# Kernel tuning notes

Measured on AMD Instinct MI355X. Metric: run time of the kernel, lower is better.

Reference implementation:

```python
import jax, jax.numpy as jnp
import numpy as np

N_NODES = 100_000
N_EDGES = 3_200_000
IN_FEATS, N_HIDDEN, N_CLASSES = 512, 64, 32
ALPHA = 0.1
NITER = 10


def setup_inputs() -> dict:
    key = jax.random.key(0)
    kx, kw1, kw2, kr, kc = jax.random.split(key, 5)
    x = jax.random.normal(kx, (N_NODES, IN_FEATS), dtype=jnp.float32)
    w1 = jax.random.normal(kw1, (N_HIDDEN, IN_FEATS), dtype=jnp.float32) / np.sqrt(IN_FEATS)
    w2 = jax.random.normal(kw2, (N_CLASSES, N_HIDDEN), dtype=jnp.float32) / np.sqrt(N_HIDDEN)
    # random edges + self loops (A + I in calc_A_hat)
    r = jax.random.randint(kr, (N_EDGES,), 0, N_NODES, dtype=jnp.int32)
    c = jax.random.randint(kc, (N_EDGES,), 0, N_NODES, dtype=jnp.int32)
    loop = jnp.arange(N_NODES, dtype=jnp.int32)
    rows = jnp.concatenate([r, loop])
    cols = jnp.concatenate([c, loop])
    # symmetric-normalization values: (1-alpha) / sqrt(d[r]*d[c]); self loops guarantee d>=1
    deg = jax.ops.segment_sum(jnp.ones_like(rows, dtype=jnp.float32), rows, num_segments=N_NODES)
    vals = (1.0 - ALPHA) / jnp.sqrt(deg[rows] * deg[cols])
    return {"x": x, "w1": w1, "w2": w2, "rows": rows, "cols": cols, "vals": vals}


def reference(x, w1, w2, rows, cols, vals):
    n = x.shape[0]
    # 2-layer bias-free MLP (dropout is identity with drop_prob=None)
    h = jnp.tanh(x @ w1.T)                 # [N, H]
    local = h @ w2.T                       # [N, C]

    def spmm(p):
        # A_hat @ p via gather-multiply-scatter over the edge list
        return jax.ops.segment_sum(vals[:, None] * p[cols], rows, num_segments=n)

    def body(p, _):
        return spmm(p) + ALPHA * local, None

    preds, _ = jax.lax.scan(body, local, None, length=NITER)
    return preds
```

## Files before the change

### kernel.cpp

```cpp
#include <hip/hip_runtime.h>
#include <math.h>

#define IN_F 512
#define NH   64
#define NC   32
#define PPR_ALPHA 0.1f
#define NITER 10

#define CH        8192
#define RPB       64
#define RPB_SHIFT 6
#define BK_PAD    1792
#define SCAP      4096

typedef _Float16 half8 __attribute__((ext_vector_type(8)));
typedef _Float16 half4 __attribute__((ext_vector_type(4)));
typedef float f32x4 __attribute__((ext_vector_type(4)));

#define XP 40

__global__ __launch_bounds__(256) void k_mlp1(const float* __restrict__ x,
                                              const float* __restrict__ w1,
                                              float* __restrict__ h, int N) {
    __shared__ _Float16 xs[64 * XP] __attribute__((aligned(16)));
    __shared__ _Float16 wsd[64 * XP] __attribute__((aligned(16)));

    const int tid = threadIdx.x;
    const int wv  = tid >> 6;
    const int l   = tid & 63;
    const int n0  = blockIdx.x * 64;

    f32x4 acc[4];
#pragma unroll
    for (int ht = 0; ht < 4; ++ht) acc[ht] = (f32x4){0.f, 0.f, 0.f, 0.f};

    const int f4 = tid & 7;
    const int r0 = tid >> 3;

    const int m  = l & 15;
    const int kg = l >> 4;

    for (int kt = 0; kt < IN_F / 32; ++kt) {
        const int k0 = kt * 32;
        __syncthreads();
#pragma unroll
        for (int qq = 0; qq < 2; ++qq) {
            const int r = r0 + 32 * qq;
            int row = n0 + r; if (row >= N) row = N - 1;
            const float4 v = *(const float4*)(x + (size_t)row * IN_F + k0 + f4 * 4);
            half4 hv; hv[0] = (_Float16)v.x; hv[1] = (_Float16)v.y;
            hv[2] = (_Float16)v.z; hv[3] = (_Float16)v.w;
            *(half4*)&xs[r * XP + f4 * 4] = hv;
        }
#pragma unroll
        for (int qq = 0; qq < 2; ++qq) {
            const int hh = r0 + 32 * qq;
            const float4 v = *(const float4*)(w1 + (size_t)hh * IN_F + k0 + f4 * 4);
            half4 hv; hv[0] = (_Float16)v.x; hv[1] = (_Float16)v.y;
            hv[2] = (_Float16)v.z; hv[3] = (_Float16)v.w;
            *(half4*)&wsd[hh * XP + f4 * 4] = hv;
        }
        __syncthreads();

        const half8 a = *(const half8*)&xs[(wv * 16 + m) * XP + kg * 8];
#pragma unroll
        for (int ht = 0; ht < 4; ++ht) {
            const half8 b = *(const half8*)&wsd[(ht * 16 + m) * XP + kg * 8];
            acc[ht] = __builtin_amdgcn_mfma_f32_16x16x32_f16(a, b, acc[ht], 0, 0, 0);
        }
    }

    const int m4 = (l >> 4) * 4;
    const int hc = l & 15;
#pragma unroll
    for (int ht = 0; ht < 4; ++ht) {
#pragma unroll
        for (int rg = 0; rg < 4; ++rg) {
            const int row = n0 + wv * 16 + m4 + rg;
            if (row < N) h[(size_t)row * NH + ht * 16 + hc] = tanhf(acc[ht][rg]);
        }
    }
}

__global__ __launch_bounds__(256) void k_mlp2(const float* __restrict__ h,
                                              const float* __restrict__ w2,
                                              const float* __restrict__ s,
                                              float* __restrict__ local,
                                              _Float16* __restrict__ q0, int N) {
    __shared__ float w2s[32 * 68];
    const int tid = threadIdx.x;
    {
        const int c = tid >> 3, f4 = tid & 7;
        *(float4*)&w2s[c * 68 + f4 * 4]       = *(const float4*)(w2 + c * NH + f4 * 4);
        *(float4*)&w2s[c * 68 + (f4 + 8) * 4] = *(const float4*)(w2 + c * NH + (f4 + 8) * 4);
    }
    __syncthreads();
    const int c = tid & 31, nl = tid >> 5;
    const int n = blockIdx.x * 8 + nl;
    if (n >= N) return;
    float acc = 0.f;
#pragma unroll
    for (int h4 = 0; h4 < NH / 4; ++h4) {
        const float4 hv = *(const float4*)(h + (size_t)n * NH + h4 * 4);
        const float4 wv = *(const float4*)&w2s[c * 68 + h4 * 4];
        acc += hv.x * wv.x + hv.y * wv.y + hv.z * wv.z + hv.w * wv.w;
    }
    local[(size_t)n * NC + c] = acc;
    q0[(size_t)n * NC + c] = (_Float16)(acc * s[n]);
}

__global__ __launch_bounds__(256) void k_p1(const int* __restrict__ rows,
                                            const int* __restrict__ cols,
                                            const float* __restrict__ vals,
                                            float* __restrict__ s,
                                            int* __restrict__ M,
                                            int E, int nb, int nCh) {
    __shared__ int lh[BK_PAD];
    const int t = threadIdx.x;
    for (int i = t; i < BK_PAD; i += 256) lh[i] = 0;
    __syncthreads();
    const int base = blockIdx.x * CH;
    const int cE = min(CH, E - base);
    for (int i = t; i < cE; i += 256) {
        const int e = base + i;
        const int r = rows[e];
        atomicAdd(&lh[r >> RPB_SHIFT], 1);
        if (r == cols[e]) s[r] = sqrtf(vals[e] * (1.0f / (1.0f - PPR_ALPHA)));
    }
    __syncthreads();
    for (int b = t; b < nb; b += 256) M[(size_t)b * nCh + blockIdx.x] = lh[b];
}

__global__ __launch_bounds__(256) void k_bsum(const int* __restrict__ in,
                                              int* __restrict__ bsum, int L) {
    __shared__ int sdata[256];
    const int t = threadIdx.x;
    const int i = blockIdx.x * 256 + t;
    sdata[t] = (i < L) ? in[i] : 0;
    __syncthreads();
    for (int off = 128; off > 0; off >>= 1) {
        if (t < off) sdata[t] += sdata[t + off];
        __syncthreads();
    }
    if (t == 0) bsum[blockIdx.x] = sdata[0];
}

__global__ __launch_bounds__(1024) void k_scanb4(int* __restrict__ bsum, int NB) {
    __shared__ int sdata[1024];
    const int t = threadIdx.x;
    const int b0 = t * 4;
    int v[4], pre[4];
    int run = 0;
#pragma unroll
    for (int j = 0; j < 4; ++j) v[j] = (b0 + j < NB) ? bsum[b0 + j] : 0;
#pragma unroll
    for (int j = 0; j < 4; ++j) { pre[j] = run; run += v[j]; }
    sdata[t] = run;
    __syncthreads();
    for (int off = 1; off < 1024; off <<= 1) {
        const int add = (t >= off) ? sdata[t - off] : 0;
        __syncthreads();
        sdata[t] += add;
        __syncthreads();
    }
    const int base = sdata[t] - run;
#pragma unroll
    for (int j = 0; j < 4; ++j)
        if (b0 + j < NB) bsum[b0 + j] = base + pre[j];
}

__global__ __launch_bounds__(256) void k_scanf(const int* __restrict__ in,
                                               const int* __restrict__ bsum,
                                               int* __restrict__ S, int L) {
    __shared__ int sdata[256];
    const int t = threadIdx.x;
    const int i = blockIdx.x * 256 + t;
    const int v = (i < L) ? in[i] : 0;
    sdata[t] = v;
    __syncthreads();
    for (int off = 1; off < 256; off <<= 1) {
        const int add = (t >= off) ? sdata[t - off] : 0;
        __syncthreads();
        sdata[t] += add;
        __syncthreads();
    }
    if (i < L) S[i] = sdata[t] - v + bsum[blockIdx.x];
}

__global__ __launch_bounds__(256) void k_bin(const int* __restrict__ rows,
                                             const int* __restrict__ cols,
                                             const int* __restrict__ S,
                                             unsigned int* __restrict__ ep,
                                             int E, int nb, int nCh) {
    __shared__ unsigned int psorted[CH];
    __shared__ unsigned short sbuck[CH];
    __shared__ int bufA[BK_PAD];
    __shared__ int lstart[BK_PAD];
    __shared__ int tsum[256];

    const int t = threadIdx.x;
    const int chunk = blockIdx.x;
    const int base = chunk * CH;
    const int cE = min(CH, E - base);

    for (int i = t; i < BK_PAD; i += 256) bufA[i] = 0;
    __syncthreads();
    for (int i = t; i < cE; i += 256)
        atomicAdd(&bufA[rows[base + i] >> RPB_SHIFT], 1);
    __syncthreads();

    {
        const int b0 = t * 7;
        int pre[7];
        int run = 0;
#pragma unroll
        for (int j = 0; j < 7; ++j) { pre[j] = run; run += bufA[b0 + j]; }
        tsum[t] = run;
        __syncthreads();
        for (int off = 1; off < 256; off <<= 1) {
            const int add = (t >= off) ? tsum[t - off] : 0;
            __syncthreads();
            tsum[t] += add;
            __syncthreads();
        }
        const int ex = tsum[t] - run;
#pragma unroll
        for (int j = 0; j < 7; ++j) {
            const int vv = ex + pre[j];
            lstart[b0 + j] = vv;
            bufA[b0 + j] = vv;
        }
    }
    __syncthreads();

    for (int i = t; i < cE; i += 256) {
        const int e = base + i;
        const int r = rows[e];
        const int b = r >> RPB_SHIFT;
        const int pos = atomicAdd(&bufA[b], 1);
        psorted[pos] = ((unsigned)(r & (RPB - 1)) << 17) | (unsigned)cols[e];
        sbuck[pos] = (unsigned short)b;
    }
    __syncthreads();

    for (int b = t; b < nb; b += 256) bufA[b] = S[(size_t)b * nCh + chunk];
    __syncthreads();

    for (int i = t; i < cE; i += 256) {
        const int b = sbuck[i];
        ep[bufA[b] + (i - lstart[b])] = psorted[i];
    }
}

__global__ __launch_bounds__(256) void k_sort2(const unsigned int* __restrict__ ep,
                                               const int* __restrict__ S,
                                               unsigned int* __restrict__ ep2,
                                               int* __restrict__ rp,
                                               int E, int N, int nb, int nCh) {
    __shared__ unsigned int buf[SCAP];
    __shared__ unsigned int srt[SCAP];
    __shared__ int cnt[RPB];
    __shared__ int cur[RPB];

    const int t = threadIdx.x;
    const int b = blockIdx.x;
    const int estart = S[(size_t)b * nCh];
    const int eend = (b + 1 < nb) ? S[(size_t)(b + 1) * nCh] : E;
    const int ne = eend - estart;

    if (t < RPB) cnt[t] = 0;
    __syncthreads();
    for (int i = t; i < ne; i += 256) {
        const unsigned u = ep[estart + i];
        buf[i] = u;
        atomicAdd(&cnt[u >> 17], 1);
    }
    __syncthreads();
    if (t < RPB) {
        const int v = cnt[t];
        int x = v;
#pragma unroll
        for (int off = 1; off < RPB; off <<= 1) {
            const int y = __shfl_up(x, off);
            if (t >= off) x += y;
        }
        const int ex = x - v;
        cur[t] = ex;
        const int idx = b * RPB + t;
        if (idx <= N) rp[idx] = estart + ex;
    }
    __syncthreads();
    for (int i = t; i < ne; i += 256) {
        const unsigned u = buf[i];
        const int r = (int)(u >> 17);
        const int pos = atomicAdd(&cur[r], 1);
        srt[pos] = u & 0x1FFFFu;
    }
    __syncthreads();
    for (int i = t; i < ne; i += 256) ep2[estart + i] = srt[i];
}

__global__ __launch_bounds__(256) void k_spmm(const int* __restrict__ rp,
                                              const unsigned int* __restrict__ ep2,
                                              const _Float16* __restrict__ q,
                                              const float* __restrict__ localv,
                                              const float* __restrict__ s,
                                              _Float16* __restrict__ dstH,
                                              float* __restrict__ dstF,
                                              int N, int storeQ) {
    const int row = blockIdx.x * 8 + (threadIdx.x >> 5);
    if (row >= N) return;
    const int lane = threadIdx.x & 31;
    const int g  = lane >> 3;
    const int cq = lane & 7;
    const int e0 = rp[row], e1 = rp[row + 1];
    const int last = e1 - 1;

    float4 a0 = {0.f, 0.f, 0.f, 0.f};
    float4 a1 = {0.f, 0.f, 0.f, 0.f};
    float4 a2 = {0.f, 0.f, 0.f, 0.f};
    float4 a3 = {0.f, 0.f, 0.f, 0.f};
    const int nIter = (e1 - e0 + 15) >> 4;
    for (int it = 0; it < nIter; ++it) {
        const int eA = e0 + it * 16 + g;
        const int eB = eA + 4, eC = eA + 8, eD = eA + 12;
        const unsigned cA = __builtin_nontemporal_load(&ep2[(eA < e1) ? eA : last]);
        const unsigned cB = __builtin_nontemporal_load(&ep2[(eB < e1) ? eB : last]);
        const unsigned cC = __builtin_nontemporal_load(&ep2[(eC < e1) ? eC : last]);
        const unsigned cD = __builtin_nontemporal_load(&ep2[(eD < e1) ? eD : last]);
        const half4 vA = *(const half4*)(q + (size_t)cA * NC + cq * 4);
        const half4 vB = *(const half4*)(q + (size_t)cB * NC + cq * 4);
        const half4 vC = *(const half4*)(q + (size_t)cC * NC + cq * 4);
        const half4 vD = *(const half4*)(q + (size_t)cD * NC + cq * 4);
        const float mA = (eA < e1) ? 1.f : 0.f;
        const float mB = (eB < e1) ? 1.f : 0.f;
        const float mC = (eC < e1) ? 1.f : 0.f;
        const float mD = (eD < e1) ? 1.f : 0.f;
        a0.x = fmaf(mA, (float)vA[0], a0.x); a0.y = fmaf(mA, (float)vA[1], a0.y);
        a0.z = fmaf(mA, (float)vA[2], a0.z); a0.w = fmaf(mA, (float)vA[3], a0.w);
        a1.x = fmaf(mB, (float)vB[0], a1.x); a1.y = fmaf(mB, (float)vB[1], a1.y);
        a1.z = fmaf(mB, (float)vB[2], a1.z); a1.w = fmaf(mB, (float)vB[3], a1.w);
        a2.x = fmaf(mC, (float)vC[0], a2.x); a2.y = fmaf(mC, (float)vC[1], a2.y);
        a2.z = fmaf(mC, (float)vC[2], a2.z); a2.w = fmaf(mC, (float)vC[3], a2.w);
        a3.x = fmaf(mD, (float)vD[0], a3.x); a3.y = fmaf(mD, (float)vD[1], a3.y);
        a3.z = fmaf(mD, (float)vD[2], a3.z); a3.w = fmaf(mD, (float)vD[3], a3.w);
    }
    float4 acc;
    acc.x = (a0.x + a1.x) + (a2.x + a3.x);
    acc.y = (a0.y + a1.y) + (a2.y + a3.y);
    acc.z = (a0.z + a1.z) + (a2.z + a3.z);
    acc.w = (a0.w + a1.w) + (a2.w + a3.w);
#pragma unroll
    for (int mask = 8; mask <= 16; mask <<= 1) {
        acc.x += __shfl_xor(acc.x, mask);
        acc.y += __shfl_xor(acc.y, mask);
        acc.z += __shfl_xor(acc.z, mask);
        acc.w += __shfl_xor(acc.w, mask);
    }
    if (g == 0) {
        const float sr = s[row];
        const float sc = (1.0f - PPR_ALPHA) * sr;
        const float4 lv = *(const float4*)(localv + (size_t)row * NC + cq * 4);
        float4 o;
        o.x = sc * acc.x + PPR_ALPHA * lv.x;
        o.y = sc * acc.y + PPR_ALPHA * lv.y;
        o.z = sc * acc.z + PPR_ALPHA * lv.z;
        o.w = sc * acc.w + PPR_ALPHA * lv.w;
        if (storeQ) {
            half4 oh;
            oh[0] = (_Float16)(o.x * sr); oh[1] = (_Float16)(o.y * sr);
            oh[2] = (_Float16)(o.z * sr); oh[3] = (_Float16)(o.w * sr);
            *(half4*)(dstH + (size_t)row * NC + cq * 4) = oh;
        } else {
            *(float4*)(dstF + (size_t)row * NC + cq * 4) = o;
        }
    }
}

extern "C" void kernel_launch(void* const* d_in, const int* in_sizes, int n_in,
                              void* d_out, int out_size, void* d_ws, size_t ws_size,
                              hipStream_t stream) {
    const float* x    = (const float*)d_in[0];
    const float* w1   = (const float*)d_in[1];
    const float* w2   = (const float*)d_in[2];
    const int*   rows = (const int*)d_in[3];
    const int*   cols = (const int*)d_in[4];
    const float* vals = (const float*)d_in[5];

    const int N = in_sizes[0] / IN_F;
    const int E = in_sizes[3];
    const int nb  = (N + RPB - 1) >> RPB_SHIFT;
    const int nCh = (E + CH - 1) / CH;
    const int L   = nb * nCh;
    const int LB  = (L + 255) / 256;

    auto align16 = [](size_t v) { return (v + 15) & ~(size_t)15; };
    char* ws = (char*)d_ws;

    const size_t szH  = align16((size_t)N * NH * 4);
    const size_t szEp = align16((size_t)E * 4);
    const size_t szM  = align16((size_t)L * 4);
    const size_t szBs = align16((size_t)LB * 4);
    const size_t szQh = align16((size_t)N * NC * 2);
    const size_t szA  = (szH > szEp) ? szH : szEp;

    float*        hbuf = (float*)ws;
    unsigned int* ep   = (unsigned int*)ws;
    size_t off = szA;
    int*          M    = (int*)(ws + off);          off += szM;
    int*          bsum = (int*)(ws + off);          off += szBs;
    unsigned int* ep2  = (unsigned int*)(ws + off); off += szEp;
    float*        localb = (float*)(ws + off);      off += align16((size_t)N * NC * 4);
    _Float16*     qA   = (_Float16*)(ws + off);     off += szQh;
    _Float16*     qB   = (_Float16*)(ws + off);     off += szQh;
    float*        sbuf = (float*)(ws + off);        off += align16((size_t)N * 4);
    int*          rp   = (int*)(ws + off);          off += align16((size_t)(N + 1) * 4);
    (void)ws_size; (void)n_in; (void)out_size;

    k_mlp1<<<(N + 63) / 64, 256, 0, stream>>>(x, w1, hbuf, N);
    k_p1<<<nCh, 256, 0, stream>>>(rows, cols, vals, sbuf, M, E, nb, nCh);
    k_mlp2<<<(N + 7) / 8, 256, 0, stream>>>(hbuf, w2, sbuf, localb, qA, N);

    k_bsum<<<LB, 256, 0, stream>>>(M, bsum, L);
    k_scanb4<<<1, 1024, 0, stream>>>(bsum, LB);
    k_scanf<<<LB, 256, 0, stream>>>(M, bsum, M, L);
    k_bin<<<nCh, 256, 0, stream>>>(rows, cols, M, ep, E, nb, nCh);
    k_sort2<<<nb, 256, 0, stream>>>(ep, M, ep2, rp, E, N, nb, nCh);

    float* outp = (float*)d_out;
    const int spmm_grid = (N + 7) / 8;
    _Float16* st[2] = {qA, qB};
    int cur = 0;
    for (int it = 1; it <= NITER; ++it) {
        const _Float16* src = st[cur];
        if (it < NITER) {
            k_spmm<<<spmm_grid, 256, 0, stream>>>(rp, ep2, src, localb, sbuf,
                                                  st[cur ^ 1], nullptr, N, 1);
        } else {
            k_spmm<<<spmm_grid, 256, 0, stream>>>(rp, ep2, src, localb, sbuf,
                                                  nullptr, outp, N, 0);
        }
        cur ^= 1;
    }
}
```

Baseline: 973.1 us.

## Stage block edge indices in LDS and widen SpMM gather unroll to eight

Each SpMM block now loads its 8 rows' contiguous column-index range into shared memory with coalesced loads, then the per-row gathers read indices from LDS instead of global memory. There is a global-memory fallback when a block has more than 1536 edges. The inner loop issues eight independent half4 gathers per iteration instead of four, and the s/localv loads are hoisted ahead of the loop to overlap latency. The cost is an extra sync and LDS usage per block, plus more registers for the eight accumulators, which may reduce occupancy.

Result: no change. 960.2 us (-1.3%).

```diff
diff --git a/kernel.cpp b/kernel.cpp
--- a/kernel.cpp
+++ b/kernel.cpp
@@ -12,6 +12,7 @@
 #define RPB_SHIFT 6
 #define BK_PAD    1792
 #define SCAP      4096
+#define ECAP      1536
 
 typedef _Float16 half8 __attribute__((ext_vector_type(8)));
 typedef _Float16 half4 __attribute__((ext_vector_type(4)));
@@ -300,6 +301,30 @@
     for (int i = t; i < ne; i += 256) ep2[estart + i] = srt[i];
 }
 
+#define SPMM_BODY(IDX_EXPR)                                                   \
+    for (int it = 0; it < nIter; ++it) {                                      \
+        const int base = l0 + it * 32 + g;                                    \
+        unsigned cc[8]; float mm[8];                                          \
+        _Pragma("unroll")                                                     \
+        for (int k = 0; k < 8; ++k) {                                         \
+            const int e = base + k * 4;                                       \
+            const int pc = (e < l1) ? e : last;                               \
+            mm[k] = (e < l1) ? 1.f : 0.f;                                     \
+            cc[k] = (IDX_EXPR);                                               \
+        }                                                                     \
+        half4 vv[8];                                                          \
+        _Pragma("unroll")                                                     \
+        for (int k = 0; k < 8; ++k)                                           \
+            vv[k] = *(const half4*)(q + (size_t)cc[k] * NC + cq * 4);         \
+        _Pragma("unroll")                                                     \
+        for (int k = 0; k < 8; ++k) {                                         \
+            a[k].x = fmaf(mm[k], (float)vv[k][0], a[k].x);                    \
+            a[k].y = fmaf(mm[k], (float)vv[k][1], a[k].y);                    \
+            a[k].z = fmaf(mm[k], (float)vv[k][2], a[k].z);                    \
+            a[k].w = fmaf(mm[k], (float)vv[k][3], a[k].w);                    \
+        }                                                                     \
+    }
+
 __global__ __launch_bounds__(256) void k_spmm(const int* __restrict__ rp,
                                               const unsigned int* __restrict__ ep2,
                                               const _Float16* __restrict__ q,
@@ -308,48 +333,52 @@
                                               _Float16* __restrict__ dstH,
                                               float* __restrict__ dstF,
                                               int N, int storeQ) {
-    const int row = blockIdx.x * 8 + (threadIdx.x >> 5);
+    __shared__ unsigned int eps[ECAP];
+    __shared__ int rps[9];
+
+    const int t = threadIdx.x;
+    const int row0 = blockIdx.x * 8;
+    if (t < 9) {
+        int rr = row0 + t;
+        rps[t] = rp[(rr <= N) ? rr : N];
+    }
+    __syncthreads();
+    const int eb0 = rps[0];
+    const int ne  = rps[8] - eb0;
+    const int nst = (ne < ECAP) ? ne : ECAP;
+    for (int i = t; i < nst; i += 256) eps[i] = ep2[eb0 + i];
+    __syncthreads();
+
+    const int grp = t >> 5;
+    const int row = row0 + grp;
     if (row >= N) return;
-    const int lane = threadIdx.x & 31;
+    const int lane = t & 31;
     const int g  = lane >> 3;
     const int cq = lane & 7;
-    const int e0 = rp[row], e1 = rp[row + 1];
-    const int last = e1 - 1;
-
-    float4 a0 = {0.f, 0.f, 0.f, 0.f};
-    float4 a1 = {0.f, 0.f, 0.f, 0.f};
-    float4 a2 = {0.f, 0.f, 0.f, 0.f};
-    float4 a3 = {0.f, 0.f, 0.f, 0.f};
-    const int nIter = (e1 - e0 + 15) >> 4;
-    for (int it = 0; it < nIter; ++it) {
-        const int eA = e0 + it * 16 + g;
-        const int eB = eA + 4, eC = eA + 8, eD = eA + 12;
-        const unsigned cA = __builtin_nontemporal_load(&ep2[(eA < e1) ? eA : last]);
-        const unsigned cB = __builtin_nontemporal_load(&ep2[(eB < e1) ? eB : last]);
-        const unsigned cC = __builtin_nontemporal_load(&ep2[(eC < e1) ? eC : last]);
-        const unsigned cD = __builtin_nontemporal_load(&ep2[(eD < e1) ? eD : last]);
-        const half4 vA = *(const half4*)(q + (size_t)cA * NC + cq * 4);
-        const half4 vB = *(const half4*)(q + (size_t)cB * NC + cq * 4);
-        const half4 vC = *(const half4*)(q + (size_t)cC * NC + cq * 4);
-        const half4 vD = *(const half4*)(q + (size_t)cD * NC + cq * 4);
-        const float mA = (eA < e1) ? 1.f : 0.f;
-        const float mB = (eB < e1) ? 1.f : 0.f;
-        const float mC = (eC < e1) ? 1.f : 0.f;
-        const float mD = (eD < e1) ? 1.f : 0.f;
-        a0.x = fmaf(mA, (float)vA[0], a0.x); a0.y = fmaf(mA, (float)vA[1], a0.y);
-        a0.z = fmaf(mA, (float)vA[2], a0.z); a0.w = fmaf(mA, (float)vA[3], a0.w);
-        a1.x = fmaf(mB, (float)vB[0], a1.x); a1.y = fmaf(mB, (float)vB[1], a1.y);
-        a1.z = fmaf(mB, (float)vB[2], a1.z); a1.w = fmaf(mB, (float)vB[3], a1.w);
-        a2.x = fmaf(mC, (float)vC[0], a2.x); a2.y = fmaf(mC, (float)vC[1], a2.y);
-        a2.z = fmaf(mC, (float)vC[2], a2.z); a2.w = fmaf(mC, (float)vC[3], a2.w);
-        a3.x = fmaf(mD, (float)vD[0], a3.x); a3.y = fmaf(mD, (float)vD[1], a3.y);
-        a3.z = fmaf(mD, (float)vD[2], a3.z); a3.w = fmaf(mD, (float)vD[3], a3.w);
-    }
+    const int l0 = rps[grp]     - eb0;
+    const int l1 = rps[grp + 1] - eb0;
+    const int last = l1 - 1;
+
+    const float sr = s[row];
+    float4 lv = {0.f, 0.f, 0.f, 0.f};
+    if (g == 0) lv = *(const float4*)(localv + (size_t)row * NC + cq * 4);
+
+    float4 a[8];
+#pragma unroll
+    for (int k = 0; k < 8; ++k) a[k] = make_float4(0.f, 0.f, 0.f, 0.f);
+
+    const int nIter = (l1 - l0 + 31) >> 5;
+    if (ne <= ECAP) {
+        SPMM_BODY(eps[pc])
+    } else {
+        SPMM_BODY(ep2[eb0 + pc])
+    }
+
     float4 acc;
-    acc.x = (a0.x + a1.x) + (a2.x + a3.x);
-    acc.y = (a0.y + a1.y) + (a2.y + a3.y);
-    acc.z = (a0.z + a1.z) + (a2.z + a3.z);
-    acc.w = (a0.w + a1.w) + (a2.w + a3.w);
+    acc.x = ((a[0].x + a[1].x) + (a[2].x + a[3].x)) + ((a[4].x + a[5].x) + (a[6].x + a[7].x));
+    acc.y = ((a[0].y + a[1].y) + (a[2].y + a[3].y)) + ((a[4].y + a[5].y) + (a[6].y + a[7].y));
+    acc.z = ((a[0].z + a[1].z) + (a[2].z + a[3].z)) + ((a[4].z + a[5].z) + (a[6].z + a[7].z));
+    acc.w = ((a[0].w + a[1].w) + (a[2].w + a[3].w)) + ((a[4].w + a[5].w) + (a[6].w + a[7].w));
 #pragma unroll
     for (int mask = 8; mask <= 16; mask <<= 1) {
         acc.x += __shfl_xor(acc.x, mask);
@@ -358,9 +387,7 @@
         acc.w += __shfl_xor(acc.w, mask);
     }
     if (g == 0) {
-        const float sr = s[row];
         const float sc = (1.0f - PPR_ALPHA) * sr;
-        const float4 lv = *(const float4*)(localv + (size_t)row * NC + cq * 4);
         float4 o;
         o.x = sc * acc.x + PPR_ALPHA * lv.x;
         o.y = sc * acc.y + PPR_ALPHA * lv.y;
```
